# Optimization experiments

Hardware: AMD Instinct MI355X
Metric: run time of the kernel (lower is better)

The kernel has to match this reference:

```python
import jax, jax.numpy as jnp
import numpy as np

N = 50000
E_RAND = 800000
IN, HID, OUT = 128, 64, 40
HEADS = (2, 1, 1)
NEG_SLOPE = 0.2


def setup_inputs() -> dict:
    key = jax.random.key(0)
    ks = jax.random.split(key, 16)
    # random edges with src != dst, then append self-loops (remove+add_self_loop)
    src_r = jax.random.randint(ks[0], (E_RAND,), 0, N)
    off = jax.random.randint(ks[1], (E_RAND,), 1, N)
    dst_r = (src_r + off) % N
    loops = jnp.arange(N)
    src = jnp.concatenate([src_r, loops]).astype(jnp.int64)
    dst = jnp.concatenate([dst_r, loops]).astype(jnp.int64)
    in_feat = jax.random.normal(ks[2], (N, IN), dtype=jnp.float32)

    def lin(k, fan_in, fan_out):
        return jax.random.normal(k, (fan_in, fan_out), dtype=jnp.float32) / np.sqrt(fan_in)

    H0, H1, H2 = HEADS
    # layer 0: in=IN, out=HID, heads=H0
    W0 = lin(ks[3], IN, H0 * HID)
    al0 = jax.random.normal(ks[4], (H0, HID), dtype=jnp.float32) * 0.1
    ar0 = jax.random.normal(ks[5], (H0, HID), dtype=jnp.float32) * 0.1
    b0 = jnp.zeros((H0 * HID,), dtype=jnp.float32)
    # layer 1: in=HID*H0, out=HID, heads=H1
    W1 = lin(ks[6], HID * H0, H1 * HID)
    al1 = jax.random.normal(ks[7], (H1, HID), dtype=jnp.float32) * 0.1
    ar1 = jax.random.normal(ks[8], (H1, HID), dtype=jnp.float32) * 0.1
    b1 = jnp.zeros((H1 * HID,), dtype=jnp.float32)
    # layer 2: in=HID*H1, out=OUT, heads=H2
    W2 = lin(ks[9], HID * H1, H2 * OUT)
    al2 = jax.random.normal(ks[10], (H2, OUT), dtype=jnp.float32) * 0.1
    ar2 = jax.random.normal(ks[11], (H2, OUT), dtype=jnp.float32) * 0.1
    b2 = jnp.zeros((H2 * OUT,), dtype=jnp.float32)
    return {"in_feat": in_feat, "src": src, "dst": dst,
            "W0": W0, "al0": al0, "ar0": ar0, "b0": b0,
            "W1": W1, "al1": al1, "ar1": ar1, "b1": b1,
            "W2": W2, "al2": al2, "ar2": ar2, "b2": b2}


def _gat_layer(x, src, dst, W, al, ar, b):
    # x: [N, Fin]; W: [Fin, H*D]; al/ar: [H, D]; b: [H*D]
    H, D = al.shape
    feat = (x @ W).reshape(-1, H, D)                 # [N, H, D]
    el = jnp.sum(feat * al, axis=-1)                 # [N, H]
    er = jnp.sum(feat * ar, axis=-1)                 # [N, H]
    e = jax.nn.leaky_relu(el[src] + er[dst], NEG_SLOPE)  # [E, H]
    m = jax.ops.segment_max(e, dst, num_segments=x.shape[0])
    ee = jnp.exp(e - jax.lax.stop_gradient(m)[dst])
    s = jax.ops.segment_sum(ee, dst, num_segments=x.shape[0])
    alpha = ee / s[dst]                              # softmax over in-edges per dst
    out = jax.ops.segment_sum(feat[src] * alpha[:, :, None], dst,
                              num_segments=x.shape[0])  # [N, H, D]
    return out + b.reshape(1, H, D)


def reference(in_feat, src, dst, W0, al0, ar0, b0, W1, al1, ar1, b1, W2, al2, ar2, b2):
    h = _gat_layer(in_feat, src, dst, W0, al0, ar0, b0).reshape(in_feat.shape[0], -1)  # flatten(1)
    h = _gat_layer(h, src, dst, W1, al1, ar1, b1).mean(axis=1)                          # mean over heads
    h = _gat_layer(h, src, dst, W2, al2, ar2, b2).reshape(in_feat.shape[0], -1)         # flatten(1)
    return h
```

## Files before the change

### kernel.cpp

```cpp
#include <hip/hip_runtime.h>
#include <hip/hip_fp16.h>
#include <math.h>

#define NEG_SLOPE 0.2f


__device__ inline float2 up2(unsigned u) {
    __half2 h;
    __builtin_memcpy(&h, &u, 4);
    return __half22float2(h);
}
__device__ inline unsigned pk2(float a, float b) {
    __half2 h = __floats2half2_rn(a, b);
    unsigned u;
    __builtin_memcpy(&u, &h, 4);
    return u;
}
__device__ inline void fma8(float* acc, const uint4& v, float p) {
    float2 f;
    f = up2(v.x); acc[0] += f.x * p; acc[1] += f.y * p;
    f = up2(v.y); acc[2] += f.x * p; acc[3] += f.y * p;
    f = up2(v.z); acc[4] += f.x * p; acc[5] += f.y * p;
    f = up2(v.w); acc[6] += f.x * p; acc[7] += f.y * p;
}
__device__ inline void fma4(float4& a, const float4& w, float xs) {
    a.x += w.x * xs; a.y += w.y * xs; a.z += w.z * xs; a.w += w.w * xs;
}
__device__ inline float dot4(const float4& a, const float4& b) {
    return a.x * b.x + a.y * b.y + a.z * b.z + a.w * b.w;
}


__global__ __launch_bounds__(256) void degree_hist_rank(const int* __restrict__ dst,
                                                        int* __restrict__ deg,
                                                        int* __restrict__ rank, int E) {
    int e = blockIdx.x * blockDim.x + threadIdx.x;
    if (e >= E) return;
    int d = __builtin_nontemporal_load(&dst[e]);
    int r = atomicAdd(&deg[d], 1);
    __builtin_nontemporal_store(r, &rank[e]);
}

__global__ __launch_bounds__(256) void scan_block_sums(const int* __restrict__ in,
                                                       int* __restrict__ partial, int n) {
    int i = blockIdx.x * 256 + threadIdx.x;
    int v = (i < n) ? in[i] : 0;
#pragma unroll
    for (int off = 32; off; off >>= 1) v += __shfl_xor(v, off);
    __shared__ int wsum[4];
    if ((threadIdx.x & 63) == 0) wsum[threadIdx.x >> 6] = v;
    __syncthreads();
    if (threadIdx.x == 0) partial[blockIdx.x] = wsum[0] + wsum[1] + wsum[2] + wsum[3];
}

__global__ __launch_bounds__(256) void scan_offsets(const int* __restrict__ partial,
                                                    int* __restrict__ partial_scan,
                                                    int* __restrict__ total_out, int nb,
                                                    const float* __restrict__ W2,
                                                    const float* __restrict__ al2,
                                                    const float* __restrict__ ar2,
                                                    float* __restrict__ W2p,
                                                    float* __restrict__ al2p,
                                                    float* __restrict__ ar2p) {
    __shared__ int buf[256];
    int t = threadIdx.x;
    int v = (t < nb) ? partial[t] : 0;
    buf[t] = v;
    __syncthreads();
    for (int off = 1; off < 256; off <<= 1) {
        int x = (t >= off) ? buf[t - off] : 0;
        __syncthreads();
        buf[t] += x;
        __syncthreads();
    }
    partial_scan[t] = buf[t] - v;
    if (t == 255) *total_out = buf[255];
    for (int i = t; i < 64 * 64; i += 256) {
        int r = i >> 6, c = i & 63;
        W2p[i] = (c < 40) ? W2[r * 40 + c] : 0.f;
    }
    if (t < 64) {
        al2p[t] = (t < 40) ? al2[t] : 0.f;
        ar2p[t] = (t < 40) ? ar2[t] : 0.f;
    }
}

__global__ __launch_bounds__(256) void scan_final(const int* __restrict__ in,
                                                  const int* __restrict__ partial_scan,
                                                  int* __restrict__ out, int n) {
    __shared__ int buf[256];
    int t = threadIdx.x;
    int i = blockIdx.x * 256 + t;
    int v = (i < n) ? in[i] : 0;
    buf[t] = v;
    __syncthreads();
    for (int off = 1; off < 256; off <<= 1) {
        int x = (t >= off) ? buf[t - off] : 0;
        __syncthreads();
        buf[t] += x;
        __syncthreads();
    }
    if (i < n) out[i] = partial_scan[blockIdx.x] + buf[t] - v;
}

__global__ __launch_bounds__(256) void scatter_rank(const int* __restrict__ src,
                                                    const int* __restrict__ dst,
                                                    const int* __restrict__ rank,
                                                    const int* __restrict__ row_start,
                                                    int* __restrict__ csr_src, int E) {
    int e = blockIdx.x * blockDim.x + threadIdx.x;
    if (e >= E) return;
    int d = __builtin_nontemporal_load(&dst[e]);
    int s = __builtin_nontemporal_load(&src[e]);
    int r = __builtin_nontemporal_load(&rank[e]);
    csr_src[row_start[d] + r] = s;
}


template <int K, int M, int G, int RPG, int H, int FSTRIDE>
__global__ __launch_bounds__((M / 4) * G) void gemm_feat_lds(const float* __restrict__ x,
                                                             const float* __restrict__ W,
                                                             const float* __restrict__ al,
                                                             const float* __restrict__ ar,
                                                             __half* __restrict__ outh,
                                                             float* __restrict__ el,
                                                             float* __restrict__ er, int N) {
    constexpr int CT = M / 4;
    constexpr int NT = CT * G;
    constexpr int ROWS = G * RPG;
    constexpr int KC = 32;
    constexpr int KC4 = KC / 4;
    constexpr int NCH = K / KC;
    constexpr int LPH = 16;
    static_assert(CT % LPH == 0, "CT must be a multiple of 16");
    __shared__ float4 sx[ROWS][KC4 + 1];
    __shared__ float4 sw[KC][CT];
    const int tid = threadIdx.x;
    const int col4 = tid % CT;
    const int grp = tid / CT;
    const int h = col4 / LPH;
    const float4* __restrict__ W4 = (const float4*)W;
    const float4* __restrict__ x4 = (const float4*)x;
    const float4 av = ((const float4*)al)[col4];
    const float4 rv = ((const float4*)ar)[col4];

    for (int base = blockIdx.x * ROWS; base < N; base += gridDim.x * ROWS) {
        float4 acc[RPG];
#pragma unroll
        for (int rr = 0; rr < RPG; ++rr) acc[rr] = float4{0.f, 0.f, 0.f, 0.f};

        for (int ch = 0; ch < NCH; ++ch) {
            __syncthreads();
#pragma unroll
            for (int i = tid; i < KC * CT; i += NT)
                sw[i / CT][i % CT] = W4[(size_t)(ch * KC) * CT + i];
#pragma unroll
            for (int i = tid; i < ROWS * KC4; i += NT) {
                int r = i / KC4, c = i % KC4;
                int row = base + r;
                sx[r][c] = (row < N) ? x4[(size_t)row * (K / 4) + ch * KC4 + c]
                                     : float4{0.f, 0.f, 0.f, 0.f};
            }
            __syncthreads();
#pragma unroll
            for (int k4 = 0; k4 < KC4; ++k4) {
                float4 w0 = sw[4 * k4 + 0][col4];
                float4 w1 = sw[4 * k4 + 1][col4];
                float4 w2 = sw[4 * k4 + 2][col4];
                float4 w3 = sw[4 * k4 + 3][col4];
#pragma unroll
                for (int rr = 0; rr < RPG; ++rr) {
                    float4 xv = sx[grp * RPG + rr][k4];
                    fma4(acc[rr], w0, xv.x);
                    fma4(acc[rr], w1, xv.y);
                    fma4(acc[rr], w2, xv.z);
                    fma4(acc[rr], w3, xv.w);
                }
            }
        }
#pragma unroll
        for (int rr = 0; rr < RPG; ++rr) {
            int row = base + grp * RPG + rr;
            if (row < N) {
                uint2 pkd;
                pkd.x = pk2(acc[rr].x, acc[rr].y);
                pkd.y = pk2(acc[rr].z, acc[rr].w);
                ((uint2*)(outh + (size_t)row * FSTRIDE))[col4] = pkd;
            }
        }
#pragma unroll
        for (int rr = 0; rr < RPG; ++rr) {
            float pl = dot4(acc[rr], av);
            float pr = dot4(acc[rr], rv);
#pragma unroll
            for (int off = 1; off < LPH; off <<= 1) {
                pl += __shfl_xor(pl, off);
                pr += __shfl_xor(pr, off);
            }
            if ((col4 % LPH) == 0) {
                int row = base + grp * RPG + rr;
                if (row < N) {
                    el[(size_t)row * H + h] = pl;
                    er[(size_t)row * H + h] = pr;
                }
            }
        }
    }
}


template <int H, int D, int FSTRIDE, int T>
__global__ __launch_bounds__(256) void gat_aggregate(const __half* __restrict__ feat,
                                                     const float* __restrict__ el,
                                                     const float* __restrict__ er,
                                                     const int* __restrict__ row_start,
                                                     const int* __restrict__ csr_src,
                                                     const float* __restrict__ bias,
                                                     float* __restrict__ out, int N) {
    constexpr int NLp = FSTRIDE / 8;
    constexpr int Gn = 64 / NLp;
    constexpr int BATCH = Gn * T;
    constexpr int WL = (H * D) / 8;
    static_assert(BATCH <= 64 && 64 % NLp == 0, "layout");
    int dstn = (blockIdx.x * blockDim.x + threadIdx.x) >> 6;
    int lane = threadIdx.x & 63;
    if (dstn >= N) return;
    int beg = row_start[dstn], end = row_start[dstn + 1];
    int cnt = end - beg;

    float er_d[H];
#pragma unroll
    for (int h = 0; h < H; ++h) er_d[h] = er[(size_t)dstn * H + h];

    float ssum[H];
    float acc8[8];
#pragma unroll
    for (int h = 0; h < H; ++h) ssum[h] = 0.f;
#pragma unroll
    for (int i = 0; i < 8; ++i) acc8[i] = 0.f;

    const int g = lane / NLp;
    const int ln = lane % NLp;

    auto gather = [&](int s_reg, const float p_reg[H], int j, int limit) {
        uint4 v[T];
#pragma unroll
        for (int t = 0; t < T; ++t) {
            if (j + Gn * t < limit) {
                int sj = __shfl(s_reg, j + Gn * t + g);
                v[t] = ((const uint4*)(feat + (size_t)sj * FSTRIDE))[ln];
            }
        }
#pragma unroll
        for (int t = 0; t < T; ++t) {
            if (j + Gn * t < limit) {
                int slot = j + Gn * t + g;
                float pj = __shfl(p_reg[0], slot);
                if constexpr (H == 2) {
                    float pj1 = __shfl(p_reg[1], slot);
                    pj = (ln >= 8) ? pj1 : pj;
                }
                fma8(acc8, v[t], pj);
            }
        }
    };

    if (cnt <= 64) {
        int idx = beg + lane;
        bool valid = idx < end;
        int s = valid ? csr_src[idx] : csr_src[beg];
        float ev[H], p[H];
        if constexpr (H == 2) {
            float2 e2 = ((const float2*)el)[s];
            ev[0] = e2.x + er_d[0];
            ev[1] = e2.y + er_d[1];
        } else {
            ev[0] = el[s] + er_d[0];
        }
#pragma unroll
        for (int h = 0; h < H; ++h) {
            float e = ev[h];
            e = (e > 0.f) ? e : NEG_SLOPE * e;
            p[h] = valid ? __expf(e) : 0.f;
            ssum[h] = p[h];
        }
        for (int j = 0; j < cnt; j += BATCH) gather(s, p, j, cnt);
    } else {
        for (int base = beg; base < end; base += 64) {
            int idx = base + lane;
            bool valid = idx < end;
            int s = valid ? csr_src[idx] : csr_src[beg];
            float p[H];
            float ev[H];
            if constexpr (H == 2) {
                float2 e2 = ((const float2*)el)[s];
                ev[0] = e2.x + er_d[0];
                ev[1] = e2.y + er_d[1];
            } else {
                ev[0] = el[s] + er_d[0];
            }
#pragma unroll
            for (int h = 0; h < H; ++h) {
                float e = ev[h];
                e = (e > 0.f) ? e : NEG_SLOPE * e;
                p[h] = valid ? __expf(e) : 0.f;
                ssum[h] += p[h];
            }
            int ccnt = (end - base < 64) ? end - base : 64;
            for (int j = 0; j < ccnt; j += BATCH) gather(s, p, j, ccnt);
        }
    }

#pragma unroll
    for (int h = 0; h < H; ++h)
#pragma unroll
        for (int off = 32; off; off >>= 1) ssum[h] += __shfl_xor(ssum[h], off);
#pragma unroll
    for (int i = 0; i < 8; ++i) {
#pragma unroll
        for (int off = NLp; off < 64; off <<= 1) acc8[i] += __shfl_xor(acc8[i], off);
    }
    if (lane < WL) {
        float inv;
        if constexpr (H == 2) inv = 1.f / ((lane >= 8) ? ssum[1] : ssum[0]);
        else inv = 1.f / ssum[0];
        float4* op = (float4*)(out + (size_t)dstn * (H * D));
        const float4* bp = (const float4*)bias;
        float4 bv0 = bp[2 * lane], bv1 = bp[2 * lane + 1];
        float4 o0, o1;
        o0.x = acc8[0] * inv + bv0.x; o0.y = acc8[1] * inv + bv0.y;
        o0.z = acc8[2] * inv + bv0.z; o0.w = acc8[3] * inv + bv0.w;
        o1.x = acc8[4] * inv + bv1.x; o1.y = acc8[5] * inv + bv1.y;
        o1.z = acc8[6] * inv + bv1.z; o1.w = acc8[7] * inv + bv1.w;
        op[2 * lane] = o0;
        op[2 * lane + 1] = o1;
    }
}


extern "C" void kernel_launch(void* const* d_in, const int* in_sizes, int n_in,
                              void* d_out, int out_size, void* d_ws, size_t ws_size,
                              hipStream_t stream) {
    const float* in_feat = (const float*)d_in[0];
    const int*   src     = (const int*)d_in[1];
    const int*   dst     = (const int*)d_in[2];
    const float* W0 = (const float*)d_in[3];
    const float* al0 = (const float*)d_in[4];
    const float* ar0 = (const float*)d_in[5];
    const float* b0 = (const float*)d_in[6];
    const float* W1 = (const float*)d_in[7];
    const float* al1 = (const float*)d_in[8];
    const float* ar1 = (const float*)d_in[9];
    const float* b1 = (const float*)d_in[10];
    const float* W2 = (const float*)d_in[11];
    const float* al2 = (const float*)d_in[12];
    const float* ar2 = (const float*)d_in[13];
    const float* b2 = (const float*)d_in[14];
    float* out = (float*)d_out;

    const int N = in_sizes[0] / 128;
    const int E = in_sizes[1];

    char* ws = (char*)d_ws;
    auto alloc = [&](size_t bytes) -> void* {
        void* p = (void*)ws;
        ws += (bytes + 255) & ~(size_t)255;
        return p;
    };
    int* deg       = (int*)alloc((size_t)N * 4);
    int* row_start = (int*)alloc((size_t)(N + 1) * 4);
    int* csr_src   = (int*)alloc((size_t)E * 4);
    int* rank      = (int*)alloc((size_t)E * 4);
    int* partial      = (int*)alloc(256 * 4);
    int* partial_scan = (int*)alloc(256 * 4);
    __half* feat   = (__half*)alloc((size_t)N * 128 * 2);
    float* el      = (float*)alloc((size_t)N * 2 * 4);
    float* er      = (float*)alloc((size_t)N * 2 * 4);
    float* h0      = (float*)alloc((size_t)N * 128 * 4);
    float* h1      = (float*)alloc((size_t)N * 64 * 4);
    float* W2p     = (float*)alloc((size_t)64 * 64 * 4);
    float* al2p    = (float*)alloc(64 * 4);
    float* ar2p    = (float*)alloc(64 * 4);

    hipMemsetAsync(deg, 0, (size_t)N * 4, stream);

    int egrid = (E + 255) / 256;
    int nb = (N + 255) / 256;

    degree_hist_rank<<<egrid, 256, 0, stream>>>(dst, deg, rank, E);
    scan_block_sums<<<nb, 256, 0, stream>>>(deg, partial, N);
    scan_offsets<<<1, 256, 0, stream>>>(partial, partial_scan, &row_start[N], nb,
                                        W2, al2, ar2, W2p, al2p, ar2p);
    scan_final<<<nb, 256, 0, stream>>>(deg, partial_scan, row_start, N);
    scatter_rank<<<egrid, 256, 0, stream>>>(src, dst, rank, row_start, csr_src, E);

    int ngrid = (N * 64 + 255) / 256;
    int ggrid32 = (N + 31) / 32;
    int ggrid64 = (N + 63) / 64;

    gemm_feat_lds<128, 128, 8, 4, 2, 128><<<ggrid32, 256, 0, stream>>>(in_feat, W0, al0, ar0, feat, el, er, N);
    gat_aggregate<2, 64, 128, 4><<<ngrid, 256, 0, stream>>>(feat, el, er, row_start, csr_src, b0, h0, N);

    gemm_feat_lds<128, 64, 16, 4, 1, 64><<<ggrid64, 256, 0, stream>>>(h0, W1, al1, ar1, feat, el, er, N);
    gat_aggregate<1, 64, 64, 4><<<ngrid, 256, 0, stream>>>(feat, el, er, row_start, csr_src, b1, h1, N);

    gemm_feat_lds<64, 64, 16, 4, 1, 64><<<ggrid64, 256, 0, stream>>>(h1, W2p, al2p, ar2p, feat, el, er, N);
    gat_aggregate<1, 40, 64, 4><<<ngrid, 256, 0, stream>>>(feat, el, er, row_start, csr_src, b2, out, N);
}
```

Before: 305.6 us.

## Use fp16 MFMA for feature GEMMs and store intermediate activations in fp16

Replaces the LDS-tiled fp32 FMA GEMMs with MFMA 16x16x32 fp16 kernels. The weights are pre-packed into the MFMA B-operand layout by a new pack kernel. The hidden activations h0/h1 are now written in fp16 by the aggregation kernels and read directly as MFMA A operands, which roughly halves that intermediate traffic. The attention logits el/er are computed from an LDS transpose of the accumulators. The cost is lower precision on the intermediates and one extra small launch.

New measurement: 283.0 us. 1.08x faster.

```diff
diff --git a/kernel.cpp b/kernel.cpp
--- a/kernel.cpp
+++ b/kernel.cpp
@@ -3,6 +3,9 @@
 #include <math.h>
 
 #define NEG_SLOPE 0.2f
+
+typedef _Float16 h8 __attribute__((ext_vector_type(8)));
+typedef float f4 __attribute__((ext_vector_type(4)));
 
 
 __device__ inline float2 up2(unsigned u) {
@@ -22,9 +25,6 @@
     f = up2(v.y); acc[2] += f.x * p; acc[3] += f.y * p;
     f = up2(v.z); acc[4] += f.x * p; acc[5] += f.y * p;
     f = up2(v.w); acc[6] += f.x * p; acc[7] += f.y * p;
-}
-__device__ inline void fma4(float4& a, const float4& w, float xs) {
-    a.x += w.x * xs; a.y += w.y * xs; a.z += w.z * xs; a.w += w.w * xs;
 }
 __device__ inline float dot4(const float4& a, const float4& b) {
     return a.x * b.x + a.y * b.y + a.z * b.z + a.w * b.w;
@@ -56,10 +56,8 @@
 __global__ __launch_bounds__(256) void scan_offsets(const int* __restrict__ partial,
                                                     int* __restrict__ partial_scan,
                                                     int* __restrict__ total_out, int nb,
-                                                    const float* __restrict__ W2,
                                                     const float* __restrict__ al2,
                                                     const float* __restrict__ ar2,
-                                                    float* __restrict__ W2p,
                                                     float* __restrict__ al2p,
                                                     float* __restrict__ ar2p) {
     __shared__ int buf[256];
@@ -75,10 +73,6 @@
     }
     partial_scan[t] = buf[t] - v;
     if (t == 255) *total_out = buf[255];
-    for (int i = t; i < 64 * 64; i += 256) {
-        int r = i >> 6, c = i & 63;
-        W2p[i] = (c < 40) ? W2[r * 40 + c] : 0.f;
-    }
     if (t < 64) {
         al2p[t] = (t < 40) ? al2[t] : 0.f;
         ar2p[t] = (t < 40) ? ar2[t] : 0.f;
@@ -117,106 +111,155 @@
 }
 
 
-template <int K, int M, int G, int RPG, int H, int FSTRIDE>
-__global__ __launch_bounds__((M / 4) * G) void gemm_feat_lds(const float* __restrict__ x,
-                                                             const float* __restrict__ W,
-                                                             const float* __restrict__ al,
-                                                             const float* __restrict__ ar,
-                                                             __half* __restrict__ outh,
-                                                             float* __restrict__ el,
-                                                             float* __restrict__ er, int N) {
-    constexpr int CT = M / 4;
-    constexpr int NT = CT * G;
-    constexpr int ROWS = G * RPG;
-    constexpr int KC = 32;
-    constexpr int KC4 = KC / 4;
-    constexpr int NCH = K / KC;
-    constexpr int LPH = 16;
-    static_assert(CT % LPH == 0, "CT must be a multiple of 16");
-    __shared__ float4 sx[ROWS][KC4 + 1];
-    __shared__ float4 sw[KC][CT];
+__global__ __launch_bounds__(256) void pack_w(const float* __restrict__ W0,
+                                              const float* __restrict__ W1,
+                                              const float* __restrict__ W2,
+                                              __half* __restrict__ P0,
+                                              __half* __restrict__ P1,
+                                              __half* __restrict__ P2) {
+    int b = blockIdx.x;
+    const float* W;
+    __half* P;
+    int K, M, Msrc;
+    if (b < 8) {
+        W = W0; P = P0; K = 128; M = 128; Msrc = 128;
+    } else if (b < 12) {
+        W = W1; P = P1; K = 128; M = 64; Msrc = 64; b -= 8;
+    } else {
+        W = W2; P = P2; K = 64; M = 64; Msrc = 40; b -= 12;
+    }
+    int t = b * 256 + threadIdx.x;
+    int nk8 = K >> 3;
+    if (t >= M * nk8) return;
+    int m = t % M, k8 = t / M;
+    int k = k8 * 8;
+    int c = m >> 4, s = k >> 5, hi = (k >> 3) & 3, lane = hi * 16 + (m & 15);
+    float v[8];
+#pragma unroll
+    for (int i = 0; i < 8; ++i)
+        v[i] = (m < Msrc) ? W[(size_t)(k + i) * Msrc + m] : 0.f;
+    uint4 o;
+    o.x = pk2(v[0], v[1]);
+    o.y = pk2(v[2], v[3]);
+    o.z = pk2(v[4], v[5]);
+    o.w = pk2(v[6], v[7]);
+    *(uint4*)(P + (size_t)((c * (K >> 5) + s) * 64 + lane) * 8) = o;
+}
+
+
+template <int K, int M, int H, bool A16>
+__global__ __launch_bounds__(256) void gemm_mfma(const void* __restrict__ xin,
+                                                 const __half* __restrict__ Wp,
+                                                 const float* __restrict__ al,
+                                                 const float* __restrict__ ar,
+                                                 __half* __restrict__ outh,
+                                                 float* __restrict__ el,
+                                                 float* __restrict__ er, int N) {
+    constexpr int KS = K / 32;
+    constexpr int CF = M / 16;
+    constexpr int LDT = 133;
+    constexpr int CH8 = M / 8;
+    constexpr int NC8 = CH8 / 4;
+    __shared__ float tl[4 * 16 * LDT];
     const int tid = threadIdx.x;
-    const int col4 = tid % CT;
-    const int grp = tid / CT;
-    const int h = col4 / LPH;
-    const float4* __restrict__ W4 = (const float4*)W;
-    const float4* __restrict__ x4 = (const float4*)x;
-    const float4 av = ((const float4*)al)[col4];
-    const float4 rv = ((const float4*)ar)[col4];
-
-    for (int base = blockIdx.x * ROWS; base < N; base += gridDim.x * ROWS) {
-        float4 acc[RPG];
-#pragma unroll
-        for (int rr = 0; rr < RPG; ++rr) acc[rr] = float4{0.f, 0.f, 0.f, 0.f};
-
-        for (int ch = 0; ch < NCH; ++ch) {
-            __syncthreads();
-#pragma unroll
-            for (int i = tid; i < KC * CT; i += NT)
-                sw[i / CT][i % CT] = W4[(size_t)(ch * KC) * CT + i];
-#pragma unroll
-            for (int i = tid; i < ROWS * KC4; i += NT) {
-                int r = i / KC4, c = i % KC4;
-                int row = base + r;
-                sx[r][c] = (row < N) ? x4[(size_t)row * (K / 4) + ch * KC4 + c]
-                                     : float4{0.f, 0.f, 0.f, 0.f};
+    const int wid = tid >> 6, lane = tid & 63;
+    const int lhi = lane >> 4, llo = lane & 15;
+    const int rowbase = blockIdx.x * 64 + wid * 16;
+    float* wt = tl + wid * 16 * LDT;
+
+    f4 acc[CF];
+#pragma unroll
+    for (int c = 0; c < CF; ++c) acc[c] = f4{0.f, 0.f, 0.f, 0.f};
+
+    const int arow = rowbase + llo;
+    const bool aval = arow < N;
+#pragma unroll
+    for (int s = 0; s < KS; ++s) {
+        h8 a = {};
+        if (aval) {
+            if constexpr (A16) {
+                const __half* xp = (const __half*)xin + (size_t)arow * K + s * 32 + lhi * 8;
+                a = *(const h8*)xp;
+            } else {
+                const float4* xp = (const float4*)((const float*)xin + (size_t)arow * K +
+                                                   s * 32 + lhi * 8);
+                float4 x0 = xp[0];
+                float4 x1 = xp[1];
+                a[0] = (_Float16)x0.x; a[1] = (_Float16)x0.y;
+                a[2] = (_Float16)x0.z; a[3] = (_Float16)x0.w;
+                a[4] = (_Float16)x1.x; a[5] = (_Float16)x1.y;
+                a[6] = (_Float16)x1.z; a[7] = (_Float16)x1.w;
             }
-            __syncthreads();
-#pragma unroll
-            for (int k4 = 0; k4 < KC4; ++k4) {
-                float4 w0 = sw[4 * k4 + 0][col4];
-                float4 w1 = sw[4 * k4 + 1][col4];
-                float4 w2 = sw[4 * k4 + 2][col4];
-                float4 w3 = sw[4 * k4 + 3][col4];
-#pragma unroll
-                for (int rr = 0; rr < RPG; ++rr) {
-                    float4 xv = sx[grp * RPG + rr][k4];
-                    fma4(acc[rr], w0, xv.x);
-                    fma4(acc[rr], w1, xv.y);
-                    fma4(acc[rr], w2, xv.z);
-                    fma4(acc[rr], w3, xv.w);
-                }
-            }
-        }
-#pragma unroll
-        for (int rr = 0; rr < RPG; ++rr) {
-            int row = base + grp * RPG + rr;
-            if (row < N) {
-                uint2 pkd;
-                pkd.x = pk2(acc[rr].x, acc[rr].y);
-                pkd.y = pk2(acc[rr].z, acc[rr].w);
-                ((uint2*)(outh + (size_t)row * FSTRIDE))[col4] = pkd;
-            }
-        }
-#pragma unroll
-        for (int rr = 0; rr < RPG; ++rr) {
-            float pl = dot4(acc[rr], av);
-            float pr = dot4(acc[rr], rv);
-#pragma unroll
-            for (int off = 1; off < LPH; off <<= 1) {
-                pl += __shfl_xor(pl, off);
-                pr += __shfl_xor(pr, off);
-            }
-            if ((col4 % LPH) == 0) {
-                int row = base + grp * RPG + rr;
-                if (row < N) {
-                    el[(size_t)row * H + h] = pl;
-                    er[(size_t)row * H + h] = pr;
-                }
-            }
-        }
-    }
-}
-
-
-template <int H, int D, int FSTRIDE, int T>
+        }
+#pragma unroll
+        for (int c = 0; c < CF; ++c) {
+            h8 b = *(const h8*)(Wp + (size_t)((c * KS + s) * 64 + lane) * 8);
+            acc[c] = __builtin_amdgcn_mfma_f32_16x16x32_f16(a, b, acc[c], 0, 0, 0);
+        }
+    }
+
+#pragma unroll
+    for (int c = 0; c < CF; ++c) {
+#pragma unroll
+        for (int r = 0; r < 4; ++r)
+            wt[(lhi * 4 + r) * LDT + c * 16 + llo] = acc[c][r];
+    }
+
+    const int rrow = lane >> 2;
+    const int q = lane & 3;
+    const int grow = rowbase + rrow;
+    float elp[H], erp[H];
+#pragma unroll
+    for (int h = 0; h < H; ++h) { elp[h] = 0.f; erp[h] = 0.f; }
+    const float4* al4 = (const float4*)al;
+    const float4* ar4 = (const float4*)ar;
+#pragma unroll
+    for (int i = 0; i < NC8; ++i) {
+        int j8 = q + 4 * i;
+        float4 v0 = *(float4*)&wt[rrow * LDT + 8 * j8];
+        float4 v1 = *(float4*)&wt[rrow * LDT + 8 * j8 + 4];
+        int h = (H == 2 && i >= NC8 / 2) ? 1 : 0;
+        float4 a0 = al4[2 * j8], a1 = al4[2 * j8 + 1];
+        float4 r0 = ar4[2 * j8], r1 = ar4[2 * j8 + 1];
+        elp[h] += dot4(v0, a0) + dot4(v1, a1);
+        erp[h] += dot4(v0, r0) + dot4(v1, r1);
+        if (grow < N) {
+            uint4 pkv;
+            pkv.x = pk2(v0.x, v0.y);
+            pkv.y = pk2(v0.z, v0.w);
+            pkv.z = pk2(v1.x, v1.y);
+            pkv.w = pk2(v1.z, v1.w);
+            *(uint4*)(outh + (size_t)grow * M + 8 * j8) = pkv;
+        }
+    }
+#pragma unroll
+    for (int h = 0; h < H; ++h) {
+#pragma unroll
+        for (int off = 1; off < 4; off <<= 1) {
+            elp[h] += __shfl_xor(elp[h], off);
+            erp[h] += __shfl_xor(erp[h], off);
+        }
+    }
+    if (q == 0 && grow < N) {
+        if constexpr (H == 2) {
+            *(float2*)&el[(size_t)grow * 2] = float2{elp[0], elp[1]};
+            *(float2*)&er[(size_t)grow * 2] = float2{erp[0], erp[1]};
+        } else {
+            el[grow] = elp[0];
+            er[grow] = erp[0];
+        }
+    }
+}
+
+
+template <int H, int D, int FSTRIDE, int T, bool OUT16>
 __global__ __launch_bounds__(256) void gat_aggregate(const __half* __restrict__ feat,
                                                      const float* __restrict__ el,
                                                      const float* __restrict__ er,
                                                      const int* __restrict__ row_start,
                                                      const int* __restrict__ csr_src,
                                                      const float* __restrict__ bias,
-                                                     float* __restrict__ out, int N) {
+                                                     void* __restrict__ out, int N) {
     constexpr int NLp = FSTRIDE / 8;
     constexpr int Gn = 64 / NLp;
     constexpr int BATCH = Gn * T;
@@ -324,7 +367,6 @@
         float inv;
         if constexpr (H == 2) inv = 1.f / ((lane >= 8) ? ssum[1] : ssum[0]);
         else inv = 1.f / ssum[0];
-        float4* op = (float4*)(out + (size_t)dstn * (H * D));
         const float4* bp = (const float4*)bias;
         float4 bv0 = bp[2 * lane], bv1 = bp[2 * lane + 1];
         float4 o0, o1;
@@ -332,8 +374,19 @@
         o0.z = acc8[2] * inv + bv0.z; o0.w = acc8[3] * inv + bv0.w;
         o1.x = acc8[4] * inv + bv1.x; o1.y = acc8[5] * inv + bv1.y;
         o1.z = acc8[6] * inv + bv1.z; o1.w = acc8[7] * inv + bv1.w;
-        op[2 * lane] = o0;
-        op[2 * lane + 1] = o1;
+        if constexpr (OUT16) {
+            __half* op = (__half*)out + (size_t)dstn * (H * D);
+            uint4 pkv;
+            pkv.x = pk2(o0.x, o0.y);
+            pkv.y = pk2(o0.z, o0.w);
+            pkv.z = pk2(o1.x, o1.y);
+            pkv.w = pk2(o1.z, o1.w);
+            ((uint4*)op)[lane] = pkv;
+        } else {
+            float4* op = (float4*)((float*)out + (size_t)dstn * (H * D));
+            op[2 * lane] = o0;
+            op[2 * lane + 1] = o1;
+        }
     }
 }
 
@@ -376,9 +429,11 @@
     __half* feat   = (__half*)alloc((size_t)N * 128 * 2);
     float* el      = (float*)alloc((size_t)N * 2 * 4);
     float* er      = (float*)alloc((size_t)N * 2 * 4);
-    float* h0      = (float*)alloc((size_t)N * 128 * 4);
-    float* h1      = (float*)alloc((size_t)N * 64 * 4);
-    float* W2p     = (float*)alloc((size_t)64 * 64 * 4);
+    __half* h0h    = (__half*)alloc((size_t)N * 128 * 2);
+    __half* h1h    = (__half*)alloc((size_t)N * 64 * 2);
+    __half* Wp0    = (__half*)alloc((size_t)128 * 128 * 2);
+    __half* Wp1    = (__half*)alloc((size_t)128 * 64 * 2);
+    __half* Wp2    = (__half*)alloc((size_t)64 * 64 * 2);
     float* al2p    = (float*)alloc(64 * 4);
     float* ar2p    = (float*)alloc(64 * 4);
 
@@ -387,23 +442,23 @@
     int egrid = (E + 255) / 256;
     int nb = (N + 255) / 256;
 
+    pack_w<<<14, 256, 0, stream>>>(W0, W1, W2, Wp0, Wp1, Wp2);
     degree_hist_rank<<<egrid, 256, 0, stream>>>(dst, deg, rank, E);
     scan_block_sums<<<nb, 256, 0, stream>>>(deg, partial, N);
     scan_offsets<<<1, 256, 0, stream>>>(partial, partial_scan, &row_start[N], nb,
-                                        W2, al2, ar2, W2p, al2p, ar2p);
+                                        al2, ar2, al2p, ar2p);
     scan_final<<<nb, 256, 0, stream>>>(deg, partial_scan, row_start, N);
     scatter_rank<<<egrid, 256, 0, stream>>>(src, dst, rank, row_start, csr_src, E);
 
     int ngrid = (N * 64 + 255) / 256;
-    int ggrid32 = (N + 31) / 32;
-    int ggrid64 = (N + 63) / 64;
-
-    gemm_feat_lds<128, 128, 8, 4, 2, 128><<<ggrid32, 256, 0, stream>>>(in_feat, W0, al0, ar0, feat, el, er, N);
-    gat_aggregate<2, 64, 128, 4><<<ngrid, 256, 0, stream>>>(feat, el, er, row_start, csr_src, b0, h0, N);
-
-    gemm_feat_lds<128, 64, 16, 4, 1, 64><<<ggrid64, 256, 0, stream>>>(h0, W1, al1, ar1, feat, el, er, N);
-    gat_aggregate<1, 64, 64, 4><<<ngrid, 256, 0, stream>>>(feat, el, er, row_start, csr_src, b1, h1, N);
-
-    gemm_feat_lds<64, 64, 16, 4, 1, 64><<<ggrid64, 256, 0, stream>>>(h1, W2p, al2p, ar2p, feat, el, er, N);
-    gat_aggregate<1, 40, 64, 4><<<ngrid, 256, 0, stream>>>(feat, el, er, row_start, csr_src, b2, out, N);
-}
+    int mgrid = (N + 63) / 64;
+
+    gemm_mfma<128, 128, 2, false><<<mgrid, 256, 0, stream>>>(in_feat, Wp0, al0, ar0, feat, el, er, N);
+    gat_aggregate<2, 64, 128, 4, true><<<ngrid, 256, 0, stream>>>(feat, el, er, row_start, csr_src, b0, h0h, N);
+
+    gemm_mfma<128, 64, 1, true><<<mgrid, 256, 0, stream>>>(h0h, Wp1, al1, ar1, feat, el, er, N);
+    gat_aggregate<1, 64, 64, 4, true><<<ngrid, 256, 0, stream>>>(feat, el, er, row_start, csr_src, b1, h1h, N);
+
+    gemm_mfma<64, 64, 1, true><<<mgrid, 256, 0, stream>>>(h1h, Wp2, al2p, ar2p, feat, el, er, N);
+    gat_aggregate<1, 40, 64, 4, false><<<ngrid, 256, 0, stream>>>(feat, el, er, row_start, csr_src, b2, out, N);
+}
```
